# Kernel tuning notes

Hardware: AMD Instinct MI355X
Metric: run time of the kernel (lower is better)

The kernel has to match this reference:

```python
import jax, jax.numpy as jnp
import numpy as np

KERNEL = 25  # hard-coded moving-average kernel in the torch Model
HID = 128


def moving_avg(x):
    # x: [B, L, C]; edge-pad (KERNEL-1)//2 on each side along time, then mean over window
    p = (KERNEL - 1) // 2
    front = jnp.repeat(x[:, 0:1, :], p, axis=1)
    end = jnp.repeat(x[:, -1:, :], p, axis=1)
    xp = jnp.concatenate([front, x, end], axis=1)  # [B, L+2p, C]
    cs = jnp.cumsum(xp, axis=1)
    cs = jnp.concatenate([jnp.zeros_like(cs[:, :1, :]), cs], axis=1)
    return (cs[:, KERNEL:, :] - cs[:, :-KERNEL, :]) / KERNEL  # [B, L, C]


def memory_enhance(repres, memory):
    # repres: [N, 128], memory: [F, 128]
    attention = jax.nn.softmax(jnp.einsum('nd,fd->nf', repres, memory), axis=1)
    output = jnp.einsum('nf,fd->nd', attention, memory)
    return jnp.concatenate([output, repres], axis=1)  # [N, 256]


def setup_inputs() -> dict:
    key = jax.random.key(0)
    ks = jax.random.split(key, 12)
    B, L, C, P, M = 128, 720, 321, 336, 512
    s = lambda k, shape, fan: jax.random.normal(k, shape, jnp.float32) * (1.0 / np.sqrt(fan))
    return {
        'x': jax.random.normal(ks[0], (B, L, C), jnp.float32),
        'W_s1': s(ks[1], (HID, L), L), 'b_s1': jnp.zeros((HID,), jnp.float32),
        'W_s2': s(ks[2], (P, 2 * HID), 2 * HID), 'b_s2': jnp.zeros((P,), jnp.float32),
        'W_t1': s(ks[3], (HID, L), L), 'b_t1': jnp.zeros((HID,), jnp.float32),
        'W_t2': s(ks[4], (P, 2 * HID), 2 * HID), 'b_t2': jnp.zeros((P,), jnp.float32),
        'mem_S': s(ks[5], (M, HID), HID),
        'mem_T': s(ks[6], (M, HID), HID),
    }


def reference(x, W_s1, b_s1, W_s2, b_s2, W_t1, b_t1, W_t2, b_t2, mem_S, mem_T):
    B, L, C = x.shape
    trend = moving_avg(x)                 # [B, L, C]
    seasonal = x - trend
    seasonal = jnp.transpose(seasonal, (0, 2, 1))  # [B, C, L]
    trend = jnp.transpose(trend, (0, 2, 1))

    def branch(init, W1, b1, mem, W2, b2):
        r = jax.nn.sigmoid(jnp.einsum('bcl,hl->bch', init, W1) + b1)  # [B, C, 128]
        r = r.reshape(-1, HID)
        r = memory_enhance(r, mem)                                    # [N, 256]
        r = r.reshape(B, C, 2 * HID)
        return jnp.einsum('bcd,pd->bcp', r, W2) + b2                  # [B, C, P]

    seasonal_out = branch(seasonal, W_s1, b_s1, mem_S, W_s2, b_s2)
    trend_out = branch(trend, W_t1, b_t1, mem_T, W_t2, b_t2)
    return jnp.transpose(seasonal_out + trend_out, (0, 2, 1))  # [B, P, C]
```

## Files before the change

kernel.cpp:

```cpp
#include <hip/hip_runtime.h>
#include <math.h>

#define BB 128
#define LL 720
#define CC 321
#define HH 128
#define PP 336
#define MM 512
#define NSTEP 23

typedef __attribute__((ext_vector_type(8))) short bf16x8;
typedef __attribute__((ext_vector_type(4))) float f32x4;

__device__ __forceinline__ short f2bf(float x) {
  unsigned u = __builtin_bit_cast(unsigned, x);
  u = (u + 0x7FFFu + ((u >> 16) & 1u)) >> 16;
  return (short)u;
}

__device__ __forceinline__ int packpos(int kw) {
  return ((kw & 15) >> 2) * 8 + (kw >> 4) * 4 + (kw & 3);
}

__device__ __forceinline__ void gload_lds16(const short* g, short* l) {
  __builtin_amdgcn_global_load_lds(
      (const __attribute__((address_space(1))) unsigned int*)g,
      (__attribute__((address_space(3))) unsigned int*)l, 16, 0, 0);
}

__global__ void weff_kernel(const float* __restrict__ Ws1,
                            const float* __restrict__ Wt1,
                            short* __restrict__ wimg) {
  int idx = blockIdx.x * 256 + threadIdx.x;
  if (idx >= HH * NSTEP * 32) return;
  int j = idx % (NSTEP * 32), h = idx / (NSTEP * 32);
  int s = j >> 5, kw = j & 31;
  int half = kw >> 4, lg = (kw >> 2) & 3, jj = kw & 3;
  size_t base = ((size_t)(s * 128 + h)) * 64 + half * 4 + jj;
  int slotS = (0 + lg) ^ (h & 7);
  int slotT = (4 + lg) ^ (h & 7);
  if (j >= LL) {
    wimg[base + slotS * 8] = 0;
    wimg[base + slotT * 8] = 0;
    return;
  }
  float ss = 0.f, st = 0.f;
  if (j == 0) {
    for (int l = 0; l <= 12; ++l) {
      float w = 13.f - (float)l;
      ss += w * Ws1[h * LL + l];
      st += w * Wt1[h * LL + l];
    }
  } else if (j == LL - 1) {
    for (int d = 0; d <= 12; ++d) {
      float w = 13.f - (float)d;
      ss += w * Ws1[h * LL + LL - 1 - d];
      st += w * Wt1[h * LL + LL - 1 - d];
    }
  } else {
    int lo = j - 12 < 0 ? 0 : j - 12;
    int hi = j + 12 > LL - 1 ? LL - 1 : j + 12;
    for (int l = lo; l <= hi; ++l) {
      ss += Ws1[h * LL + l];
      st += Wt1[h * LL + l];
    }
  }
  ss *= (1.f / 25.f);
  st *= (1.f / 25.f);
  wimg[base + slotS * 8] = f2bf(Ws1[h * LL + j] - ss);
  wimg[base + slotT * 8] = f2bf(st);
}

__global__ void xstage_kernel(const float* __restrict__ x,
                              short* __restrict__ ximg) {
  int blk = blockIdx.x, s = blockIdx.y;
  int t = threadIdx.x;
  int n = blk * 64 + t;
  int b = n / CC, c = n - b * CC;
  const float* xp = x + (size_t)b * (LL * CC) + c;
  float v[32];
  int k0 = s * 32;
#pragma unroll
  for (int kk = 0; kk < 32; ++kk) {
    int k = k0 + kk;
    v[kk] = (k < LL) ? xp[(size_t)k * CC] : 0.f;
  }
  __builtin_amdgcn_sched_barrier(0);
  short* dst = ximg + ((size_t)(blk * NSTEP + s)) * 2048;
#pragma unroll
  for (int lg = 0; lg < 4; ++lg) {
    int chunk = lg * 64 + (t ^ (2 * lg));
    union { short sv[8]; int4 q; } u;
#pragma unroll
    for (int j = 0; j < 4; ++j) {
      u.sv[j] = f2bf(v[lg * 4 + j]);
      u.sv[j + 4] = f2bf(v[16 + lg * 4 + j]);
    }
    *(int4*)&dst[chunk * 8] = u.q;
  }
}

__global__ void memstage_kernel(const float* __restrict__ memS,
                                const float* __restrict__ memT,
                                short* __restrict__ stgS,
                                short* __restrict__ stgT) {
  int e = blockIdx.x * 256 + threadIdx.x;
  int br = e >> 14;
  int s = e & 16383;
  const float* src = br ? memT : memS;
  short* dst = br ? stgT : stgS;
  int tt = s >> 11;
  int c = s & 2047;
  int row = c >> 4, slot = c & 15;
  int sp = slot ^ (row & 7);
  int k = sp >> 2, lg = sp & 3;
  int ft = tt >> 1;
  short out[8];
  if ((tt & 1) == 0) {
    const float* r0 = src + (size_t)(ft * 128 + row) * 128 + k * 32 + lg * 4;
#pragma unroll
    for (int j = 0; j < 4; ++j) {
      out[j] = f2bf(r0[j]);
      out[j + 4] = f2bf(r0[16 + j]);
    }
  } else {
    int fbase = ft * 128 + k * 32 + lg * 4;
#pragma unroll
    for (int j = 0; j < 4; ++j) {
      out[j] = f2bf(src[(size_t)(fbase + j) * 128 + row]);
      out[j + 4] = f2bf(src[(size_t)(fbase + 16 + j) * 128 + row]);
    }
  }
  short4 a = make_short4(out[0], out[1], out[2], out[3]);
  short4 b = make_short4(out[4], out[5], out[6], out[7]);
  *(short4*)&dst[(size_t)s * 8] = a;
  *(short4*)&dst[(size_t)s * 8 + 4] = b;
}

__global__ void w2cvt_kernel(const float* __restrict__ Ws2,
                             const float* __restrict__ Wt2,
                             const float* __restrict__ bs2,
                             const float* __restrict__ bt2,
                             short* __restrict__ W2b, float* __restrict__ b2) {
  int i = blockIdx.x * 256 + threadIdx.x;
  if (i < PP) b2[i] = bs2[i] + bt2[i];
  if (i >= PP * 512) return;
  int p = i >> 9, k = i & 511;
  float v = (k < 256) ? Ws2[p * 256 + k] : Wt2[p * 256 + (k - 256)];
  W2b[p * 512 + (k >> 5) * 32 + packpos(k & 31)] = f2bf(v);
}

__global__ __launch_bounds__(256) void gemm1_mfma(
    const short* __restrict__ wimg, const short* __restrict__ ximg,
    const float* __restrict__ bs1, const float* __restrict__ bt1,
    short* __restrict__ r2s, short* __restrict__ r2t) {
  __shared__ __align__(16) short wbuf[2][8192];
  __shared__ __align__(16) short xbuf[2][2048];
  int tid = threadIdx.x;
  int w = tid >> 6, l = tid & 63, lr = l & 15, lg = l >> 4;
  int br = w >> 1, hb = (w & 1) * 64;
  int blk = blockIdx.x;
  int nb = blk * 64;

  const short* wsrc = wimg + (size_t)w * 2048 + l * 8;
  const short* xsrc = ximg + (size_t)blk * NSTEP * 2048 + tid * 8;

  f32x4 acc[4][4];
#pragma unroll
  for (int i = 0; i < 4; ++i)
#pragma unroll
    for (int g = 0; g < 4; ++g) acc[i][g] = (f32x4){0.f, 0.f, 0.f, 0.f};

#define STAGE(ss, bb)                                                     \
  do {                                                                    \
    const short* ws_ = wsrc + (size_t)(ss)*8192;                          \
    _Pragma("unroll") for (int i = 0; i < 4; ++i)                         \
        gload_lds16(ws_ + i * 512, &wbuf[bb][w * 2048 + i * 512]);        \
    gload_lds16(xsrc + (size_t)(ss)*2048, &xbuf[bb][(tid & 192) * 8]);    \
  } while (0)

  STAGE(0, 0);
  __syncthreads();

  int cur = 0;
  for (int s = 0; s < NSTEP; ++s) {
    if (s < NSTEP - 1) STAGE(s + 1, cur ^ 1);

    const short* tw = &wbuf[cur][0];
    const short* tx = &xbuf[cur][0];
    bf16x8 afr[4], bfr[4];
#pragma unroll
    for (int ht = 0; ht < 4; ++ht) {
      int h = hb + ht * 16 + lr;
      int slot = (br * 4 + lg) ^ (h & 7);
      afr[ht] = *(const bf16x8*)&tw[h * 64 + slot * 8];
    }
#pragma unroll
    for (int ng = 0; ng < 4; ++ng) {
      int nl = ng * 16 + lr;
      int chunk = lg * 64 + (nl ^ (2 * lg));
      bfr[ng] = *(const bf16x8*)&tx[chunk * 8];
    }
#pragma unroll
    for (int ht = 0; ht < 4; ++ht)
#pragma unroll
      for (int ng = 0; ng < 4; ++ng)
        acc[ht][ng] = __builtin_amdgcn_mfma_f32_16x16x32_bf16(
            afr[ht], bfr[ng], acc[ht][ng], 0, 0, 0);

    __syncthreads();
    cur ^= 1;
  }
#undef STAGE

  const float* bias = br ? bt1 : bs1;
  short* r2 = br ? r2t : r2s;
#pragma unroll
  for (int ht = 0; ht < 4; ++ht) {
    int h0 = hb + ht * 16 + lg * 4;
    int dst = (h0 >> 5) * 32 + lg * 8 + ((h0 >> 4) & 1) * 4;
    float4 bi4 = *(const float4*)&bias[h0];
    const float* pb = &bi4.x;
#pragma unroll
    for (int ng = 0; ng < 4; ++ng) {
      int n = nb + ng * 16 + lr;
      short4 v;
      short* pv = &v.x;
#pragma unroll
      for (int j = 0; j < 4; ++j)
        pv[j] = f2bf(1.f / (1.f + __expf(-(acc[ht][ng][j] + pb[j]))));
      *(short4*)&r2[(size_t)n * 256 + 128 + dst] = v;
    }
  }
}

__global__ __launch_bounds__(256) void memenh_mfma(
    const short* __restrict__ stgS, const short* __restrict__ stgT,
    short* __restrict__ r2s, short* __restrict__ r2t) {
  int br = blockIdx.y;
  const short* stg = br ? stgT : stgS;
  short* r2 = br ? r2t : r2s;

  __shared__ __align__(16) short buf[2][16384];
  int tid = threadIdx.x;
  int l = tid & 63, lr = l & 15, lg = l >> 4;
  int wbase = tid & 192;
  int n = blockIdx.x * 64 + (tid >> 6) * 16 + lr;

  bf16x8 brag[4];
  {
    const short* rb = r2 + (size_t)n * 256 + 128;
#pragma unroll
    for (int k = 0; k < 4; ++k)
      brag[k] = *(const bf16x8*)&rb[k * 32 + lg * 8];
  }

#define STAGE(t, bsel)                                                        \
  {                                                                           \
    const short* g = stg + (size_t)(t)*16384;                                 \
    _Pragma("unroll") for (int i = 0; i < 8; ++i) {                           \
      gload_lds16(g + (size_t)(i * 256 + tid) * 8,                            \
                  &buf[bsel][(i * 256 + wbase) * 8]);                         \
    }                                                                         \
  }

  STAGE(0, 0);
  __syncthreads();

  f32x4 accO[8];
#pragma unroll
  for (int i = 0; i < 8; ++i) accO[i] = (f32x4){0.f, 0.f, 0.f, 0.f};
  bf16x8 pb[4];
  float ssum = 0.f;
  int cur = 0;

#pragma unroll
  for (int t = 0; t < 8; ++t) {
    if (t < 7) STAGE(t + 1, cur ^ 1);
    const short* tb = &buf[cur][0];
    if ((t & 1) == 0) {
      f32x4 sc[8];
#pragma unroll
      for (int ft16 = 0; ft16 < 8; ++ft16) {
        f32x4 a = {0.f, 0.f, 0.f, 0.f};
#pragma unroll
        for (int k = 0; k < 4; ++k) {
          int row = ft16 * 16 + lr;
          int slot = (4 * k + lg) ^ (row & 7);
          bf16x8 af = *(const bf16x8*)&tb[row * 128 + slot * 8];
          a = __builtin_amdgcn_mfma_f32_16x16x32_bf16(af, brag[k], a, 0, 0, 0);
        }
        sc[ft16] = a;
      }
#pragma unroll
      for (int i = 0; i < 8; ++i) {
        f32x4 v = sc[i];
#pragma unroll
        for (int j = 0; j < 4; ++j) {
          float e = __expf(v[j]);
          v[j] = e;
          ssum += e;
        }
        sc[i] = v;
      }
#pragma unroll
      for (int t4 = 0; t4 < 4; ++t4) {
        f32x4 e0 = sc[2 * t4], e1 = sc[2 * t4 + 1];
        bf16x8 f;
        f[0] = f2bf(e0[0]); f[1] = f2bf(e0[1]);
        f[2] = f2bf(e0[2]); f[3] = f2bf(e0[3]);
        f[4] = f2bf(e1[0]); f[5] = f2bf(e1[1]);
        f[6] = f2bf(e1[2]); f[7] = f2bf(e1[3]);
        pb[t4] = f;
      }
    } else {
#pragma unroll
      for (int dt = 0; dt < 8; ++dt) {
#pragma unroll
        for (int k = 0; k < 4; ++k) {
          int row = dt * 16 + lr;
          int slot = (4 * k + lg) ^ (row & 7);
          bf16x8 af = *(const bf16x8*)&tb[row * 128 + slot * 8];
          accO[dt] =
              __builtin_amdgcn_mfma_f32_16x16x32_bf16(af, pb[k], accO[dt], 0, 0, 0);
        }
      }
    }
    __syncthreads();
    cur ^= 1;
  }
#undef STAGE

  ssum += __shfl_xor(ssum, 16);
  ssum += __shfl_xor(ssum, 32);
  float inv = 1.f / ssum;
  short* rowO = r2 + (size_t)n * 256;
#pragma unroll
  for (int dt = 0; dt < 8; ++dt) {
    short4 o;
    o.x = f2bf(accO[dt][0] * inv);
    o.y = f2bf(accO[dt][1] * inv);
    o.z = f2bf(accO[dt][2] * inv);
    o.w = f2bf(accO[dt][3] * inv);
    *(short4*)&rowO[(dt >> 1) * 32 + lg * 8 + (dt & 1) * 4] = o;
  }
}

__global__ __launch_bounds__(512) void gemm2_mfma(
    const short* __restrict__ r2s, const short* __restrict__ r2t,
    const short* __restrict__ W2b,
    const float* __restrict__ b2,
    float* __restrict__ out) {
  __shared__ __align__(16) short w2lds[2][112 * 40];
  int tid = threadIdx.x;
  int w = tid >> 6, l = tid & 63, lr = l & 15, lg = l >> 4;
  int p0 = blockIdx.y * 112;
  int n = blockIdx.x * 128 + w * 16 + lr;
  int b = n / CC, c = n - b * CC;
  const short* rs = r2s + (size_t)n * 256;
  const short* rt = r2t + (size_t)n * 256;

  bool dostage = tid < 448;
  int row = tid >> 2, q = tid & 3;
  const short* gW = W2b + (size_t)(p0 + row) * 512 + q * 8;
  int doff = row * 40 + q * 8;

  f32x4 acc[7];
#pragma unroll
  for (int i = 0; i < 7; ++i) acc[i] = (f32x4){0.f, 0.f, 0.f, 0.f};

  if (dostage) *(int4*)&w2lds[0][doff] = *(const int4*)gW;
  __syncthreads();

  int cur = 0;
  for (int step = 0; step < 16; ++step) {
    int k0 = step * 32;
    const short* rrow = ((k0 < 256) ? rs : rt) + (k0 & 255);
    bf16x8 bfr = *(const bf16x8*)&rrow[lg * 8];
    int4 nxt = {0, 0, 0, 0};
    if (step < 15 && dostage) nxt = *(const int4*)(gW + (step + 1) * 32);
    const short* tw = &w2lds[cur][0];
#pragma unroll
    for (int pt = 0; pt < 7; ++pt) {
      bf16x8 a = *(const bf16x8*)&tw[(pt * 16 + lr) * 40 + lg * 8];
      acc[pt] = __builtin_amdgcn_mfma_f32_16x16x32_bf16(a, bfr, acc[pt], 0, 0, 0);
    }
    if (step < 15 && dostage) *(int4*)&w2lds[cur ^ 1][doff] = nxt;
    __syncthreads();
    cur ^= 1;
  }

  size_t obase = (size_t)b * ((size_t)PP * CC) + c;
#pragma unroll
  for (int pt = 0; pt < 7; ++pt) {
    int p = p0 + pt * 16 + lg * 4;
    float4 bias = *(const float4*)&b2[p];
    const float* pb = &bias.x;
#pragma unroll
    for (int j = 0; j < 4; ++j) {
      out[obase + (size_t)(p + j) * CC] = acc[pt][j] + pb[j];
    }
  }
}

extern "C" void kernel_launch(void* const* d_in, const int* in_sizes, int n_in,
                              void* d_out, int out_size, void* d_ws, size_t ws_size,
                              hipStream_t stream) {
  const float* x    = (const float*)d_in[0];
  const float* Ws1  = (const float*)d_in[1];
  const float* bs1  = (const float*)d_in[2];
  const float* Ws2  = (const float*)d_in[3];
  const float* bs2  = (const float*)d_in[4];
  const float* Wt1  = (const float*)d_in[5];
  const float* bt1  = (const float*)d_in[6];
  const float* Wt2  = (const float*)d_in[7];
  const float* bt2  = (const float*)d_in[8];
  const float* memS = (const float*)d_in[9];
  const float* memT = (const float*)d_in[10];
  float* out = (float*)d_out;

  const size_t N = (size_t)BB * CC;
  short* r2s  = (short*)d_ws;
  short* r2t  = r2s + N * 256;
  short* wimg = r2t + N * 256;
  short* stgS = wimg + (size_t)NSTEP * 128 * 64;
  short* stgT = stgS + (size_t)16384 * 8;
  short* W2b  = stgT + (size_t)16384 * 8;
  float* b2   = (float*)(W2b + (size_t)PP * 512);
  short* ximg = (short*)(b2 + PP);

  weff_kernel<<<(HH * NSTEP * 32 + 255) / 256, 256, 0, stream>>>(Ws1, Wt1, wimg);
  memstage_kernel<<<128, 256, 0, stream>>>(memS, memT, stgS, stgT);
  w2cvt_kernel<<<(PP * 512) / 256, 256, 0, stream>>>(Ws2, Wt2, bs2, bt2, W2b, b2);

  dim3 gx(642, NSTEP);
  xstage_kernel<<<gx, 64, 0, stream>>>(x, ximg);

  gemm1_mfma<<<642, 256, 0, stream>>>(wimg, ximg, bs1, bt1, r2s, r2t);

  dim3 g3(642, 2);
  memenh_mfma<<<g3, 256, 0, stream>>>(stgS, stgT, r2s, r2t);

  dim3 g2(321, 3);
  gemm2_mfma<<<g2, 512, 0, stream>>>(r2s, r2t, W2b, b2, out);
}
```

Before: 159.0 us.

## Fuse x bf16 staging into gemm1 with register-prefetched loads and padded LDS

Removes the separate xstage kernel that converted x to a bf16 image in global memory. gemm1 now reads fp32 x directly with float4 loads (handling batch-boundary crossings), converts to bf16 and writes it into a padded LDS layout, prefetching the next step in registers during the MFMAs. This cuts a kernel launch and a global write/read round trip of the staged image. The cost is scalar LDS reads to assemble B fragments and extra VGPR pressure.

```diff
diff --git a/kernel.cpp b/kernel.cpp
--- a/kernel.cpp
+++ b/kernel.cpp
@@ -69,35 +69,6 @@
   st *= (1.f / 25.f);
   wimg[base + slotS * 8] = f2bf(Ws1[h * LL + j] - ss);
   wimg[base + slotT * 8] = f2bf(st);
-}
-
-__global__ void xstage_kernel(const float* __restrict__ x,
-                              short* __restrict__ ximg) {
-  int blk = blockIdx.x, s = blockIdx.y;
-  int t = threadIdx.x;
-  int n = blk * 64 + t;
-  int b = n / CC, c = n - b * CC;
-  const float* xp = x + (size_t)b * (LL * CC) + c;
-  float v[32];
-  int k0 = s * 32;
-#pragma unroll
-  for (int kk = 0; kk < 32; ++kk) {
-    int k = k0 + kk;
-    v[kk] = (k < LL) ? xp[(size_t)k * CC] : 0.f;
-  }
-  __builtin_amdgcn_sched_barrier(0);
-  short* dst = ximg + ((size_t)(blk * NSTEP + s)) * 2048;
-#pragma unroll
-  for (int lg = 0; lg < 4; ++lg) {
-    int chunk = lg * 64 + (t ^ (2 * lg));
-    union { short sv[8]; int4 q; } u;
-#pragma unroll
-    for (int j = 0; j < 4; ++j) {
-      u.sv[j] = f2bf(v[lg * 4 + j]);
-      u.sv[j + 4] = f2bf(v[16 + lg * 4 + j]);
-    }
-    *(int4*)&dst[chunk * 8] = u.q;
-  }
 }
 
 __global__ void memstage_kernel(const float* __restrict__ memS,
@@ -151,19 +122,53 @@
 }
 
 __global__ __launch_bounds__(256) void gemm1_mfma(
-    const short* __restrict__ wimg, const short* __restrict__ ximg,
+    const float* __restrict__ x, const short* __restrict__ wimg,
     const float* __restrict__ bs1, const float* __restrict__ bt1,
     short* __restrict__ r2s, short* __restrict__ r2t) {
   __shared__ __align__(16) short wbuf[2][8192];
-  __shared__ __align__(16) short xbuf[2][2048];
+  __shared__ __align__(16) short xbuf[2][2304];
   int tid = threadIdx.x;
   int w = tid >> 6, l = tid & 63, lr = l & 15, lg = l >> 4;
   int br = w >> 1, hb = (w & 1) * 64;
-  int blk = blockIdx.x;
-  int nb = blk * 64;
+  int nb = blockIdx.x * 64;
 
   const short* wsrc = wimg + (size_t)w * 2048 + l * 8;
-  const short* xsrc = ximg + (size_t)blk * NSTEP * 2048 + tid * 8;
+
+  const float* cbase[2];
+  int coff[2][4];
+  bool ccross[2];
+  int ckk[2], cdst[2];
+#pragma unroll
+  for (int i = 0; i < 2; ++i) {
+    int e = tid + i * 256;
+    int kk = e >> 4, c4 = e & 15;
+    ckk[i] = kk;
+    int n0 = nb + c4 * 4;
+    int b0 = n0 / CC, c0 = n0 - b0 * CC;
+    cbase[i] = x + (size_t)b0 * (LL * CC) + c0;
+    ccross[i] = (c0 + 3 >= CC);
+#pragma unroll
+    for (int j = 0; j < 4; ++j)
+      coff[i][j] = j + ((c0 + j >= CC) ? (LL - 1) * CC : 0);
+    cdst[i] = (c4 & 3) * 4 + (kk & 3) * 16 + ((kk >> 2) & 3) * 72 +
+              (kk >> 4) * 288 + (c4 >> 2) * 576;
+  }
+
+#define XLOAD(i, s_, out)                                                  \
+  do {                                                                     \
+    int k_ = (s_)*32 + ckk[i];                                             \
+    if (k_ < LL) {                                                         \
+      if (!ccross[i]) {                                                    \
+        float4 t4 = *(const float4*)(cbase[i] + (size_t)k_ * CC);          \
+        out[0] = t4.x; out[1] = t4.y; out[2] = t4.z; out[3] = t4.w;        \
+      } else {                                                             \
+        _Pragma("unroll") for (int j = 0; j < 4; ++j)                      \
+            out[j] = cbase[i][(size_t)k_ * CC + coff[i][j]];               \
+      }                                                                    \
+    } else {                                                               \
+      out[0] = out[1] = out[2] = out[3] = 0.f;                             \
+    }                                                                      \
+  } while (0)
 
   f32x4 acc[4][4];
 #pragma unroll
@@ -171,20 +176,33 @@
 #pragma unroll
     for (int g = 0; g < 4; ++g) acc[i][g] = (f32x4){0.f, 0.f, 0.f, 0.f};
 
-#define STAGE(ss, bb)                                                     \
-  do {                                                                    \
-    const short* ws_ = wsrc + (size_t)(ss)*8192;                          \
-    _Pragma("unroll") for (int i = 0; i < 4; ++i)                         \
-        gload_lds16(ws_ + i * 512, &wbuf[bb][w * 2048 + i * 512]);        \
-    gload_lds16(xsrc + (size_t)(ss)*2048, &xbuf[bb][(tid & 192) * 8]);    \
-  } while (0)
-
-  STAGE(0, 0);
+  {
+    float xv0[4], xv1[4];
+    XLOAD(0, 0, xv0);
+    XLOAD(1, 0, xv1);
+#pragma unroll
+    for (int i = 0; i < 4; ++i)
+      gload_lds16(wsrc + i * 512, &wbuf[0][w * 2048 + i * 512]);
+    short4 s0 = make_short4(f2bf(xv0[0]), f2bf(xv0[1]), f2bf(xv0[2]),
+                            f2bf(xv0[3]));
+    short4 s1 = make_short4(f2bf(xv1[0]), f2bf(xv1[1]), f2bf(xv1[2]),
+                            f2bf(xv1[3]));
+    *(short4*)&xbuf[0][cdst[0]] = s0;
+    *(short4*)&xbuf[0][cdst[1]] = s1;
+  }
   __syncthreads();
 
   int cur = 0;
   for (int s = 0; s < NSTEP; ++s) {
-    if (s < NSTEP - 1) STAGE(s + 1, cur ^ 1);
+    float xn0[4], xn1[4];
+    if (s < NSTEP - 1) {
+      XLOAD(0, s + 1, xn0);
+      XLOAD(1, s + 1, xn1);
+      const short* ws = wsrc + (size_t)(s + 1) * 8192;
+#pragma unroll
+      for (int i = 0; i < 4; ++i)
+        gload_lds16(ws + i * 512, &wbuf[cur ^ 1][w * 2048 + i * 512]);
+    }
 
     const short* tw = &wbuf[cur][0];
     const short* tx = &xbuf[cur][0];
@@ -197,9 +215,14 @@
     }
 #pragma unroll
     for (int ng = 0; ng < 4; ++ng) {
-      int nl = ng * 16 + lr;
-      int chunk = lg * 64 + (nl ^ (2 * lg));
-      bfr[ng] = *(const bf16x8*)&tx[chunk * 8];
+      int base0 = lr + lg * 72 + ng * 576;
+      bf16x8 f;
+#pragma unroll
+      for (int j = 0; j < 4; ++j) {
+        f[j] = tx[base0 + j * 16];
+        f[j + 4] = tx[base0 + j * 16 + 288];
+      }
+      bfr[ng] = f;
     }
 #pragma unroll
     for (int ht = 0; ht < 4; ++ht)
@@ -208,10 +231,18 @@
         acc[ht][ng] = __builtin_amdgcn_mfma_f32_16x16x32_bf16(
             afr[ht], bfr[ng], acc[ht][ng], 0, 0, 0);
 
+    if (s < NSTEP - 1) {
+      short4 s0 = make_short4(f2bf(xn0[0]), f2bf(xn0[1]), f2bf(xn0[2]),
+                              f2bf(xn0[3]));
+      short4 s1 = make_short4(f2bf(xn1[0]), f2bf(xn1[1]), f2bf(xn1[2]),
+                              f2bf(xn1[3]));
+      *(short4*)&xbuf[cur ^ 1][cdst[0]] = s0;
+      *(short4*)&xbuf[cur ^ 1][cdst[1]] = s1;
+    }
     __syncthreads();
     cur ^= 1;
   }
-#undef STAGE
+#undef XLOAD
 
   const float* bias = br ? bt1 : bs1;
   short* r2 = br ? r2t : r2s;
@@ -427,16 +458,12 @@
   short* stgT = stgS + (size_t)16384 * 8;
   short* W2b  = stgT + (size_t)16384 * 8;
   float* b2   = (float*)(W2b + (size_t)PP * 512);
-  short* ximg = (short*)(b2 + PP);
 
   weff_kernel<<<(HH * NSTEP * 32 + 255) / 256, 256, 0, stream>>>(Ws1, Wt1, wimg);
   memstage_kernel<<<128, 256, 0, stream>>>(memS, memT, stgS, stgT);
   w2cvt_kernel<<<(PP * 512) / 256, 256, 0, stream>>>(Ws2, Wt2, bs2, bt2, W2b, b2);
 
-  dim3 gx(642, NSTEP);
-  xstage_kernel<<<gx, 64, 0, stream>>>(x, ximg);
-
-  gemm1_mfma<<<642, 256, 0, stream>>>(wimg, ximg, bs1, bt1, r2s, r2t);
+  gemm1_mfma<<<642, 256, 0, stream>>>(x, wimg, bs1, bt1, r2s, r2t);
 
   dim3 g3(642, 2);
   memenh_mfma<<<g3, 256, 0, stream>>>(stgS, stgT, r2s, r2t);
```

Result: faster. 151.1 us (-5.0%).
